# Optimization experiments

Measured on AMD Instinct MI355X. Metric: run time of the kernel, lower is better.

Reference implementation:

```python
import jax, jax.numpy as jnp
import numpy as np

C = 1.2            # PoincareBall curvature (learnable in torch, init value used)
SQC = C ** 0.5
MIN_NORM = 1e-15
BALL_EPS = 4e-3    # geoopt float32 projx eps

def _artanh(x):
    return jnp.arctanh(jnp.clip(x, -1.0 + 1e-7, 1.0 - 1e-7))

def _tanh(x):
    return jnp.tanh(jnp.clip(x, -15.0, 15.0))

def _norm(x):
    return jnp.maximum(jnp.linalg.norm(x, axis=-1, keepdims=True), MIN_NORM)

def p_projx(x):
    n = _norm(x)
    maxnorm = (1.0 - BALL_EPS) / SQC
    return jnp.where(n > maxnorm, x / n * maxnorm, x)

def p_expmap0(u):
    n = _norm(u)
    return p_projx(_tanh(SQC * n) * u / (SQC * n))

def p_logmap0(y):
    n = _norm(y)
    return _artanh(SQC * n) * y / (SQC * n)

def p_mobius_add(x, y):
    x2 = jnp.sum(x * x, -1, keepdims=True)
    y2 = jnp.sum(y * y, -1, keepdims=True)
    xy = jnp.sum(x * y, -1, keepdims=True)
    num = (1 + 2 * C * xy + C * y2) * x + (1 - C * x2) * y
    den = 1 + 2 * C * xy + C * C * x2 * y2
    return num / jnp.maximum(den, MIN_NORM)

def p_mobius_matvec(W, x):
    xn = _norm(x)
    mx = x @ W.T
    mxn = _norm(mx)
    res = _tanh(mxn / xn * _artanh(SQC * xn)) * mx / (mxn * SQC)
    zero = jnp.all(mx == 0, axis=-1, keepdims=True)
    return p_projx(jnp.where(zero, jnp.zeros_like(res), res))

def p_mobius_scalar_mul(r, x):
    n = _norm(x)
    return p_projx(_tanh(r * _artanh(SQC * n)) * x / (n * SQC))

def p_linear(x, W, b):
    # Manifold_Linear on PoincareBall: mobius matvec + mobius bias add + projx
    mv = p_mobius_matvec(W, x)
    return p_projx(p_mobius_add(mv, p_expmap0(b)))

def e_linear(x, W, b):
    return x @ W.T + b

def mob_relu(x):
    # Mob_Act: logmap0 -> act -> expmap0 (with projection)
    return p_expmap0(jax.nn.relu(p_logmap0(x)))


def setup_inputs() -> dict:
    key = jax.random.key(0)
    ks = jax.random.split(key, 26)
    g = lambda i, shape, s: (jax.random.normal(ks[i], shape, jnp.float32) * s)
    d = {
        'x':   g(0, (1024, 32, 128), 1.0),
        'We1': g(1, (80, 32), 0.1),   'be1': g(2, (80,), 0.05),
        'We2': g(3, (104, 80), 0.1),  'be2': g(4, (104,), 0.05),
        'We3': g(5, (128, 104), 0.1), 'be3': g(6, (128,), 0.05),
        'Wh1': g(7, (80, 32), 0.1),   'bh1': g(8, (80,), 0.05),
        'Wh2': g(9, (104, 80), 0.1),  'bh2': g(10, (104,), 0.05),
        'Wh3': g(11, (128, 104), 0.1),'bh3': g(12, (128,), 0.05),
        'Wae': g(13, (128, 128), 0.1),'bae': g(14, (128,), 0.05),
        'Wah': g(15, (128, 128), 0.1),'bah': g(16, (128,), 0.05),
        'Wte': g(17, (1, 128), 0.1),  'bte': g(18, (1,), 0.05),
        'Wth': g(19, (1, 128), 0.1),  'bth': g(20, (1,), 0.05),
        'Wf1': g(21, (10, 256), 0.1), 'bf1': g(22, (10,), 0.05),
        'Wf2': g(23, (10, 10), 0.1),  'bf2': g(24, (10,), 0.05),
    }
    return d


def reference(x, We1, be1, We2, be2, We3, be3,
              Wh1, bh1, Wh2, bh2, Wh3, bh3,
              Wae, bae, Wah, bah, Wte, bte, Wth, bth,
              Wf1, bf1, Wf2, bf2):
    xs = jnp.transpose(x, (0, 2, 1))  # (B, S, C_in)

    # --- Euclidean branch: expmap0 = identity; Manifold_Linear = plain linear ---
    xe = xs
    xe = e_linear(xe, We1, be1); xe = jax.nn.relu(xe)
    xe = e_linear(xe, We2, be2); xe = jax.nn.relu(xe)
    xe = e_linear(xe, We3, be3)
    out_e = jax.nn.relu(xe)               # extra self.act for Euclidean manifolds

    # --- Poincare branch ---
    xh = p_expmap0(xs)
    xh = p_linear(xh, Wh1, bh1); xh = mob_relu(xh)
    xh = p_linear(xh, Wh2, bh2); xh = mob_relu(xh)
    out_h = p_linear(xh, Wh3, bh3)        # (B, S, part_dim)

    # --- cross-manifold attention in tangent space at origin ---
    tan_e = e_linear(out_e, Wae, bae)                    # Euclidean logmap0 = id
    tan_h = p_logmap0(p_linear(out_h, Wah, bah))
    mu = 0.5 * (tan_e + tan_h)
    a_e = e_linear(tan_e - mu, Wte, bte)  # (B, S, 1)
    a_h = e_linear(tan_h - mu, Wth, bth)
    w = jax.nn.softmax(jnp.stack([a_e, a_h], axis=0), axis=0)
    proc_e = w[0] * out_e                                # Euclidean mobius scalar mul
    proc_h = p_mobius_scalar_mul(w[1], out_h)

    # --- pool over constituents in tangent space, concat, classify ---
    o_e = jnp.mean(proc_e, axis=1)                       # Euclidean logmap0 = id
    o_h = jnp.mean(p_logmap0(proc_h), axis=1)
    o = jnp.concatenate([o_e, o_h], axis=-1)             # (B, 2*part_dim)
    o = jax.nn.relu(e_linear(o, Wf1, bf1))
    return e_linear(o, Wf2, bf2)
```

## Files before the change

kernel.cpp:

```cpp
#include <hip/hip_runtime.h>
#include <math.h>

constexpr float CC   = 1.2f;
constexpr float SQC  = 1.09544511501033215f;
constexpr float MAXN = (1.0f - 4e-3f) / SQC;
constexpr float MINN = 1e-15f;

constexpr int WTH1 = 0;
constexpr int WTH2 = 4096;
constexpr int WTH3 = 14336;
constexpr int WTAH = 27648;
constexpr int WTE1 = 44032;
constexpr int WTE2 = 48128;
constexpr int WTE3 = 58368;
constexpr int EB1  = 71680;
constexpr int EB2  = 71808;
constexpr int EB3  = 71936;
constexpr int EBA  = 72064;
constexpr int BE1  = 72192;
constexpr int BE2  = 72320;
constexpr int BE3  = 72448;
constexpr int U1o  = 72576;
constexpr int U2o  = 72704;
constexpr int SCo  = 72832;
constexpr int PART = 72864;

constexpr int ASTR  = 65;
constexpr int L_ACT = 0;
constexpr int L_ZH  = 8320;
constexpr int L_SCR = 8960;
constexpr int L_TOT = 9000;

__device__ __forceinline__ float art_(float x){
  x = fminf(fmaxf(x, -0.9999999f), 0.9999999f);
  return 0.5f * __logf((1.0f + x) / (1.0f - x));
}
__device__ __forceinline__ float tanh_(float x){
  x = fminf(fmaxf(x, -15.0f), 15.0f);
  float e = __expf(2.0f * x);
  return (e - 1.0f) / (e + 1.0f);
}
__device__ __forceinline__ float wsum(float v){
#pragma unroll
  for(int i=32;i>0;i>>=1) v += __shfl_xor(v, i, 64);
  return v;
}
__device__ __forceinline__ float rtj(float v){
  v += __shfl_xor(v, 1, 64); v += __shfl_xor(v, 2, 64);
  v += __shfl_xor(v, 4, 64); v += __shfl_xor(v, 8, 64);
  return v;
}
__device__ __forceinline__ float lamv(float nv){
  float n = fmaxf(nv, MINN);
  return art_(SQC*n)/(SQC*n);
}
struct HS { float ca, cb, nv; };
__device__ __forceinline__ HS hyper_chain(float m2, float meb, float xn_in, float y2){
  float xn  = fmaxf(xn_in, MINN);
  float mxn = fmaxf(sqrtf(m2), MINN);
  float r   = art_(SQC*xn);
  float s   = tanh_(mxn/xn*r)/(mxn*SQC);
  float nr  = s*mxn;
  if(nr > MAXN){ s *= MAXN/nr; nr = MAXN; }
  float xy = s*meb, x2 = nr*nr;
  float den = fmaxf(1.f + 2.f*CC*xy + CC*CC*x2*y2, MINN);
  float A   = (1.f + 2.f*CC*xy + CC*y2)/den;
  float Bc  = (1.f - CC*x2)/den;
  float n3  = sqrtf(fmaxf(A*A*x2 + 2.f*A*Bc*xy + Bc*Bc*y2, 0.f));
  float rho = (n3 > MAXN) ? MAXN/n3 : 1.f;
  HS h; h.nv = fminf(n3, MAXN); h.ca = rho*A*s; h.cb = rho*Bc;
  return h;
}
struct TT { float tau, nf; };
__device__ __forceinline__ TT tail_relu(float rn2){
  float rn = fmaxf(sqrtf(rn2), MINN);
  float th = tanh_(SQC*rn);
  TT r; r.tau = th/(SQC*rn); r.nf = th/SQC;
  if(r.nf > MAXN){ r.tau *= MAXN/r.nf; r.nf = MAXN; }
  return r;
}
struct EX { float nh, scl; };
__device__ __forceinline__ EX exp0(float n2){
  float n0 = fmaxf(sqrtf(n2), MINN);
  float th = tanh_(SQC*n0);
  EX e; e.nh = th/SQC; e.scl = th/(SQC*n0);
  if(e.nh > MAXN){ e.scl *= MAXN/e.nh; e.nh = MAXN; }
  return e;
}
struct THW { float te, th2; };
__device__ __forceinline__ THW ahchain(float m2a, float mw1, float mw2, float meba,
                                       float xnh, float rr, float y2,
                                       float ebw1, float ebw2){
  float mxn = fmaxf(sqrtf(m2a), MINN);
  float s = tanh_(mxn/xnh*rr)/(mxn*SQC);
  float nr = s*mxn;
  if(nr > MAXN){ s *= MAXN/nr; nr = MAXN; }
  float xy = s*meba, x2 = nr*nr;
  float den = fmaxf(1.f + 2.f*CC*xy + CC*CC*x2*y2, MINN);
  float A = (1.f + 2.f*CC*xy + CC*y2)/den;
  float Bc = (1.f - CC*x2)/den;
  float n3 = sqrtf(fmaxf(A*A*x2 + 2.f*A*Bc*xy + Bc*Bc*y2, 0.f));
  float rho = (n3 > MAXN) ? MAXN/n3 : 1.f;
  float nv = fminf(n3, MAXN);
  float lr = lamv(nv)*rho;
  THW r; r.te = lr*(A*s*mw1 + Bc*ebw1); r.th2 = lr*(A*s*mw2 + Bc*ebw2);
  return r;
}
struct AG { float wge, g2; };
__device__ __forceinline__ AG attn(float d1, float d2, float thte, float thth,
                                   float rr, float xnh, float b_e, float b_h){
  float a_e = 0.5f*(d1 - thte) + b_e;
  float a_h = 0.5f*(thth - d2) + b_h;
  float mx = fmaxf(a_e, a_h);
  float ee = __expf(a_e - mx), eh = __expf(a_h - mx);
  float inv = 1.f/(ee + eh);
  AG r; r.wge = ee*inv;
  float wgh = eh*inv;
  float inner = wgh*rr;
  float scl2 = tanh_(inner)/(xnh*SQC);
  float nn = scl2*xnh;
  if(nn > MAXN){ scl2 *= MAXN/nn; nn = MAXN; }
  r.g2 = lamv(nn)*scl2;
  return r;
}

__global__ void k_setup(const float* __restrict__ Wh1, const float* __restrict__ Wh2,
                        const float* __restrict__ Wh3, const float* __restrict__ Wah,
                        const float* __restrict__ We1, const float* __restrict__ We2,
                        const float* __restrict__ We3,
                        const float* __restrict__ Wae, const float* __restrict__ bae,
                        const float* __restrict__ bh1, const float* __restrict__ bh2,
                        const float* __restrict__ bh3, const float* __restrict__ bah,
                        const float* __restrict__ Wte, const float* __restrict__ Wth,
                        const float* __restrict__ be1, const float* __restrict__ be2,
                        const float* __restrict__ be3, float* __restrict__ ws){
  const int blk = blockIdx.x, tid = threadIdx.x;
  if(blk < 280){
    const int row = blk*2 + (tid >> 7);
    const int j   = tid & 127;
    const float* W; int OUT, K, kk, dst;
    if(row < 32)       { W=Wh1; OUT=80;  K=32;  kk=row;      dst=WTH1; }
    else if(row < 112) { W=Wh2; OUT=104; K=80;  kk=row-32;   dst=WTH2; }
    else if(row < 216) { W=Wh3; OUT=128; K=104; kk=row-112;  dst=WTH3; }
    else if(row < 344) { W=Wah; OUT=128; K=128; kk=row-216;  dst=WTAH; }
    else if(row < 376) { W=We1; OUT=80;  K=32;  kk=row-344;  dst=WTE1; }
    else if(row < 456) { W=We2; OUT=104; K=80;  kk=row-376;  dst=WTE2; }
    else               { W=We3; OUT=128; K=104; kk=row-456;  dst=WTE3; }
    ws[dst + kk*128 + j] = (j < OUT) ? W[j*K + kk] : 0.f;
    return;
  }
  {
    const int which = tid >> 7, k = tid & 127;
    const float* wv = which ? Wth : Wte;
    float s = 0.f;
#pragma unroll 4
    for(int j=0;j<128;++j) s += Wae[j*128+k] * wv[j];
    ws[(which ? U2o : U1o) + k] = s;
  }
  if(tid < 128){
    ws[BE1+tid] = (tid < 80)  ? be1[tid] : 0.f;
    ws[BE2+tid] = (tid < 104) ? be2[tid] : 0.f;
    ws[BE3+tid] = be3[tid];
  }
  if(tid < 64){
    const int l = tid;
    float p1=0.f, p2=0.f;
    for(int j=l;j<128;j+=64){ p1 += bae[j]*Wte[j]; p2 += bae[j]*Wth[j]; }
    p1 = wsum(p1); p2 = wsum(p2);
    if(l==0){ ws[SCo+0]=p1; ws[SCo+1]=p2; }
    const float* bs[4] = {bh1,bh2,bh3,bah};
    const int dims[4]  = {80,104,128,128};
    const int offs[4]  = {EB1,EB2,EB3,EBA};
    for(int v=0;v<4;++v){
      const float* bp = bs[v]; const int D = dims[v];
      float q = 0.f;
      for(int j=l;j<D;j+=64) q += bp[j]*bp[j];
      q = wsum(q);
      float nb = fmaxf(sqrtf(q), MINN);
      float th = tanhf(fminf(fmaxf(SQC*nb,-15.f),15.f));
      float coef = th/(SQC*nb);
      float ne = th/SQC;
      if(ne > MAXN){ coef *= MAXN/ne; ne = MAXN; }
      for(int j=l;j<D;j+=64) ws[offs[v]+j] = coef*bp[j];
      for(int j=D+l;j<128;j+=64) ws[offs[v]+j] = 0.f;
      if(l==0) ws[SCo+2+v] = ne*ne;
      if(v==3){
        float e1=0.f, e2=0.f;
        for(int j=l;j<D;j+=64){ e1 += bp[j]*Wte[j]; e2 += bp[j]*Wth[j]; }
        e1 = wsum(e1)*coef; e2 = wsum(e2)*coef;
        if(l==0){ ws[SCo+6]=e1; ws[SCo+7]=e2; }
      }
    }
  }
}

__global__ void k_fin(const float* __restrict__ ws, const float* __restrict__ bf1,
                      const float* __restrict__ Wf2, const float* __restrict__ bf2,
                      float* __restrict__ out){
  const int r = blockIdx.x*64 + threadIdx.x;
  const float* p = ws + PART + (size_t)r*20;
  float f1[10];
#pragma unroll
  for(int i=0;i<10;++i)
    f1[i] = fmaxf((p[i] + p[10+i])*(1.f/128.f) + bf1[i], 0.f);
#pragma unroll
  for(int o=0;o<10;++o){
    float a = bf2[o];
#pragma unroll
    for(int k=0;k<10;++k) a = fmaf(Wf2[o*10+k], f1[k], a);
    out[r*10 + o] = a;
  }
}

__device__ __forceinline__ void ld8(const float* __restrict__ p, float (&v)[8]){
  float4 a = *(const float4*)p, b = *(const float4*)(p+4);
  v[0]=a.x; v[1]=a.y; v[2]=a.z; v[3]=a.w; v[4]=b.x; v[5]=b.y; v[6]=b.z; v[7]=b.w;
}

template<int K, bool XG, bool XSQ>
__device__ __forceinline__ void gemm4(const float* __restrict__ wt,
                                      const float* __restrict__ xg,
                                      const float* __restrict__ ACT,
                                      int tj, int tt, float (&acc)[4][8], float (&xsq)[4]){
#pragma unroll
  for(int i=0;i<4;++i)
#pragma unroll
    for(int j=0;j<8;++j) acc[i][j] = 0.f;
  const int wo = tj*8, xo = tt*4;
#pragma unroll 4
  for(int k=0;k<K;++k){
    float4 w0 = *(const float4*)(wt + k*128 + wo);
    float4 w1 = *(const float4*)(wt + k*128 + wo + 4);
    float4 xa;
    if(XG) xa = *(const float4*)(xg + k*128 + xo);
    else   xa = *(const float4*)(ACT + k*ASTR + xo);
    float xv[4] = {xa.x,xa.y,xa.z,xa.w};
    float wv[8] = {w0.x,w0.y,w0.z,w0.w,w1.x,w1.y,w1.z,w1.w};
#pragma unroll
    for(int i=0;i<4;++i){
      if(XSQ) xsq[i] = fmaf(xv[i], xv[i], xsq[i]);
#pragma unroll
      for(int j=0;j<8;++j) acc[i][j] = fmaf(xv[i], wv[j], acc[i][j]);
    }
  }
}

__device__ __forceinline__ void wACT(float* __restrict__ ACT, const float (&acc)[4][8],
                                     int tj, int tt){
#pragma unroll
  for(int j=0;j<8;++j){
    float4 a = {acc[0][j],acc[1][j],acc[2][j],acc[3][j]};
    *(float4*)(ACT + (tj*8+j)*ASTR + tt*4) = a;
  }
}

__global__ __launch_bounds__(256, 4) void k_main(
    const float* __restrict__ x,
    const float* __restrict__ Wf1, const float* __restrict__ Wte,
    const float* __restrict__ bte, const float* __restrict__ Wth,
    const float* __restrict__ bth, float* __restrict__ ws){
  extern __shared__ float lds[];
  float* ACT = lds + L_ACT;
  float* ZH  = lds + L_ZH;
  float* SCR = lds + L_SCR;
  const int tid = threadIdx.x, tj = tid & 15, tt = tid >> 4;
  const int b = blockIdx.x, b2 = b >> 1, hf = b & 1;
  const int tok0 = tt*4;
  const float* xg = x + (size_t)b2*4096 + hf*64;

  const float c1  = ws[SCo+0], c2  = ws[SCo+1];
  const float y21 = ws[SCo+2], y22 = ws[SCo+3], y23 = ws[SCo+4], y2a = ws[SCo+5];
  const float ew1 = ws[SCo+6], ew2 = ws[SCo+7];
  const float btev = bte[0], bthv = bth[0];

  float acc[4][8];
  float xsq[4];
#pragma unroll
  for(int i=0;i<4;++i) xsq[i] = 0.f;

  float nf[4], xnh[4], rr[4], tte[4], tth[4];

  {
    gemm4<32,true,true>(ws+WTH1, xg, ACT, tj, tt, acc, xsq);
    float ebv[8]; ld8(ws+EB1+tj*8, ebv);
#pragma unroll
    for(int i=0;i<4;++i){
      float s=0.f, e=0.f;
#pragma unroll
      for(int j=0;j<8;++j){ s = fmaf(acc[i][j],acc[i][j],s); e = fmaf(acc[i][j],ebv[j],e); }
      s = rtj(s); e = rtj(e);
      EX e0 = exp0(xsq[i]);
      HS h = hyper_chain(s*e0.scl*e0.scl, e*e0.scl, e0.nh, y21);
      float lam = lamv(h.nv), ca = h.ca*e0.scl, cb = h.cb;
      float s2 = 0.f;
#pragma unroll
      for(int j=0;j<8;++j){
        float v = fmaxf(lam*fmaf(ca, acc[i][j], cb*ebv[j]), 0.f);
        acc[i][j] = v; s2 = fmaf(v,v,s2);
      }
      s2 = rtj(s2);
      TT tr = tail_relu(s2); nf[i] = tr.nf;
#pragma unroll
      for(int j=0;j<8;++j) acc[i][j] *= tr.tau;
    }
    wACT(ACT, acc, tj, tt);
    __syncthreads();
  }

  {
    gemm4<80,false,false>(ws+WTH2, nullptr, ACT, tj, tt, acc, xsq);
    float ebv[8]; ld8(ws+EB2+tj*8, ebv);
#pragma unroll
    for(int i=0;i<4;++i){
      float s=0.f, e=0.f;
#pragma unroll
      for(int j=0;j<8;++j){ s = fmaf(acc[i][j],acc[i][j],s); e = fmaf(acc[i][j],ebv[j],e); }
      s = rtj(s); e = rtj(e);
      HS h = hyper_chain(s, e, nf[i], y22);
      float lam = lamv(h.nv);
      float s2 = 0.f;
#pragma unroll
      for(int j=0;j<8;++j){
        float v = fmaxf(lam*fmaf(h.ca, acc[i][j], h.cb*ebv[j]), 0.f);
        acc[i][j] = v; s2 = fmaf(v,v,s2);
      }
      s2 = rtj(s2);
      TT tr = tail_relu(s2); nf[i] = tr.nf;
#pragma unroll
      for(int j=0;j<8;++j) acc[i][j] *= tr.tau;
    }
    __syncthreads();
    wACT(ACT, acc, tj, tt);
    __syncthreads();
  }

  {
    gemm4<104,false,false>(ws+WTH3, nullptr, ACT, tj, tt, acc, xsq);
    float ebv[8]; ld8(ws+EB3+tj*8, ebv);
#pragma unroll
    for(int i=0;i<4;++i){
      float s=0.f, e=0.f;
#pragma unroll
      for(int j=0;j<8;++j){ s = fmaf(acc[i][j],acc[i][j],s); e = fmaf(acc[i][j],ebv[j],e); }
      s = rtj(s); e = rtj(e);
      HS h = hyper_chain(s, e, nf[i], y23);
      xnh[i] = fmaxf(h.nv, MINN);
      rr[i]  = art_(SQC*xnh[i]);
#pragma unroll
      for(int j=0;j<8;++j) acc[i][j] = fmaf(h.ca, acc[i][j], h.cb*ebv[j]);
    }
    __syncthreads();
    wACT(ACT, acc, tj, tt);
#pragma unroll
    for(int ic=0;ic<10;++ic){
      float wf[8]; ld8(Wf1 + ic*256 + 128 + tj*8, wf);
#pragma unroll
      for(int i=0;i<4;++i){
        float s=0.f;
#pragma unroll
        for(int j=0;j<8;++j) s = fmaf(acc[i][j], wf[j], s);
        s = rtj(s);
        if(tj==0) ZH[ic*64 + tok0 + i] = s;
      }
    }
    __syncthreads();
  }

  {
    gemm4<128,false,false>(ws+WTAH, nullptr, ACT, tj, tt, acc, xsq);
    float w1v[8], w2v[8], eav[8];
    ld8(Wte + tj*8, w1v); ld8(Wth + tj*8, w2v); ld8(ws+EBA+tj*8, eav);
#pragma unroll
    for(int i=0;i<4;++i){
      float s0=0.f,s1=0.f,s2=0.f,s3=0.f;
#pragma unroll
      for(int j=0;j<8;++j){
        float m = acc[i][j];
        s0 = fmaf(m,m,s0); s1 = fmaf(m,w1v[j],s1);
        s2 = fmaf(m,w2v[j],s2); s3 = fmaf(m,eav[j],s3);
      }
      s0=rtj(s0); s1=rtj(s1); s2=rtj(s2); s3=rtj(s3);
      THW a = ahchain(s0, s1, s2, s3, xnh[i], rr[i], y2a, ew1, ew2);
      tte[i] = a.te; tth[i] = a.th2;
    }
  }

  {
    gemm4<32,true,false>(ws+WTE1, xg, ACT, tj, tt, acc, xsq);
    float bev[8]; ld8(ws+BE1+tj*8, bev);
#pragma unroll
    for(int i=0;i<4;++i)
#pragma unroll
      for(int j=0;j<8;++j) acc[i][j] = fmaxf(acc[i][j]+bev[j], 0.f);
    __syncthreads();
    wACT(ACT, acc, tj, tt);
    __syncthreads();
  }
  {
    gemm4<80,false,false>(ws+WTE2, nullptr, ACT, tj, tt, acc, xsq);
    float bev[8]; ld8(ws+BE2+tj*8, bev);
#pragma unroll
    for(int i=0;i<4;++i)
#pragma unroll
      for(int j=0;j<8;++j) acc[i][j] = fmaxf(acc[i][j]+bev[j], 0.f);
    __syncthreads();
    wACT(ACT, acc, tj, tt);
    __syncthreads();
  }
  {
    gemm4<104,false,false>(ws+WTE3, nullptr, ACT, tj, tt, acc, xsq);
    float bev[8], u1v[8], u2v[8];
    ld8(ws+BE3+tj*8, bev); ld8(ws+U1o+tj*8, u1v); ld8(ws+U2o+tj*8, u2v);
    float wge[4], g2v[4];
#pragma unroll
    for(int i=0;i<4;++i){
      float s1=0.f, s2=0.f;
#pragma unroll
      for(int j=0;j<8;++j){
        float v = fmaxf(acc[i][j]+bev[j], 0.f);
        acc[i][j] = v;
        s1 = fmaf(v,u1v[j],s1); s2 = fmaf(v,u2v[j],s2);
      }
      s1 = rtj(s1); s2 = rtj(s2);
      AG g = attn(s1 + c1, s2 + c2, tte[i], tth[i], rr[i], xnh[i], btev, bthv);
      wge[i] = g.wge; g2v[i] = g.g2;
    }
#pragma unroll
    for(int ic=0;ic<10;++ic){
      float wf[8]; ld8(Wf1 + ic*256 + tj*8, wf);
      float pv = 0.f;
#pragma unroll
      for(int i=0;i<4;++i){
        float z=0.f;
#pragma unroll
        for(int j=0;j<8;++j) z = fmaf(acc[i][j], wf[j], z);
        z = rtj(z);
        pv += wge[i]*z + g2v[i]*ZH[ic*64 + tok0 + i];
      }
      pv += __shfl_xor(pv, 16, 64);
      pv += __shfl_xor(pv, 32, 64);
      if((tid & 63) == 0) SCR[(tid>>6)*10 + ic] = pv;
    }
    __syncthreads();
    if(tid < 10)
      ws[PART + (size_t)b*10 + tid] =
        SCR[tid] + SCR[10+tid] + SCR[20+tid] + SCR[30+tid];
  }
}

extern "C" void kernel_launch(void* const* d_in, const int* in_sizes, int n_in,
                              void* d_out, int out_size, void* d_ws, size_t ws_size,
                              hipStream_t stream){
  (void)in_sizes; (void)n_in; (void)out_size; (void)ws_size;
  const float* x   = (const float*)d_in[0];
  const float* We1 = (const float*)d_in[1];
  const float* be1 = (const float*)d_in[2];
  const float* We2 = (const float*)d_in[3];
  const float* be2 = (const float*)d_in[4];
  const float* We3 = (const float*)d_in[5];
  const float* be3 = (const float*)d_in[6];
  const float* Wh1 = (const float*)d_in[7];
  const float* bh1 = (const float*)d_in[8];
  const float* Wh2 = (const float*)d_in[9];
  const float* bh2 = (const float*)d_in[10];
  const float* Wh3 = (const float*)d_in[11];
  const float* bh3 = (const float*)d_in[12];
  const float* Wae = (const float*)d_in[13];
  const float* bae = (const float*)d_in[14];
  const float* Wah = (const float*)d_in[15];
  const float* bah = (const float*)d_in[16];
  const float* Wte = (const float*)d_in[17];
  const float* bte = (const float*)d_in[18];
  const float* Wth = (const float*)d_in[19];
  const float* bth = (const float*)d_in[20];
  const float* Wf1 = (const float*)d_in[21];
  const float* bf1 = (const float*)d_in[22];
  const float* Wf2 = (const float*)d_in[23];
  const float* bf2 = (const float*)d_in[24];
  float* ws  = (float*)d_ws;
  float* out = (float*)d_out;

  hipLaunchKernelGGL(k_setup, dim3(281), dim3(256), 0, stream,
                     Wh1, Wh2, Wh3, Wah, We1, We2, We3,
                     Wae, bae, bh1, bh2, bh3, bah, Wte, Wth, be1, be2, be3, ws);

  const int smem = L_TOT * 4;
  hipLaunchKernelGGL(k_main, dim3(2048), dim3(256), smem, stream,
                     x, Wf1, Wte, bte, Wth, bth, ws);

  hipLaunchKernelGGL(k_fin, dim3(16), dim3(64), 0, stream,
                     ws, bf1, Wf2, bf2, out);
}
```

Measured before the change: 590.8 us.

## Double threads per block with 4x4 register tiles and lane-distributed per-token chains

Blocks grow from 256 to 512 threads. Each thread now holds a 4x4 accumulator tile instead of 4x8, so output-feature reductions span 32 lanes. The per-token hyperbolic scalar chains, which every lane used to compute for all 4 of its tokens, now run once per lane for a single selected token, and the coefficients are broadcast back with shuffles. This spreads the expensive transcendental work and cuts register pressure to allow more resident waves, at the cost of extra shuffles and a longer reduction tree.

```diff
diff --git a/kernel.cpp b/kernel.cpp
--- a/kernel.cpp
+++ b/kernel.cpp
@@ -29,7 +29,7 @@
 constexpr int L_ACT = 0;
 constexpr int L_ZH  = 8320;
 constexpr int L_SCR = 8960;
-constexpr int L_TOT = 9000;
+constexpr int L_TOT = 9040;
 
 __device__ __forceinline__ float art_(float x){
   x = fminf(fmaxf(x, -0.9999999f), 0.9999999f);
@@ -45,11 +45,19 @@
   for(int i=32;i>0;i>>=1) v += __shfl_xor(v, i, 64);
   return v;
 }
-__device__ __forceinline__ float rtj(float v){
+__device__ __forceinline__ float rtj32(float v){
   v += __shfl_xor(v, 1, 64); v += __shfl_xor(v, 2, 64);
   v += __shfl_xor(v, 4, 64); v += __shfl_xor(v, 8, 64);
+  v += __shfl_xor(v, 16, 64);
   return v;
 }
+__device__ __forceinline__ float sel4(const float (&a)[4], int i){
+  float lo = (i & 1) ? a[1] : a[0];
+  float hi = (i & 1) ? a[3] : a[2];
+  return (i & 2) ? hi : lo;
+}
+__device__ __forceinline__ float bc(float v, int src){ return __shfl(v, src, 64); }
+
 __device__ __forceinline__ float lamv(float nv){
   float n = fmaxf(nv, MINN);
   return art_(SQC*n)/(SQC*n);
@@ -212,49 +220,48 @@
   }
 }
 
-__device__ __forceinline__ void ld8(const float* __restrict__ p, float (&v)[8]){
-  float4 a = *(const float4*)p, b = *(const float4*)(p+4);
-  v[0]=a.x; v[1]=a.y; v[2]=a.z; v[3]=a.w; v[4]=b.x; v[5]=b.y; v[6]=b.z; v[7]=b.w;
+__device__ __forceinline__ void ld4(const float* __restrict__ p, float (&v)[4]){
+  float4 a = *(const float4*)p;
+  v[0]=a.x; v[1]=a.y; v[2]=a.z; v[3]=a.w;
 }
 
 template<int K, bool XG, bool XSQ>
 __device__ __forceinline__ void gemm4(const float* __restrict__ wt,
                                       const float* __restrict__ xg,
                                       const float* __restrict__ ACT,
-                                      int tj, int tt, float (&acc)[4][8], float (&xsq)[4]){
+                                      int tj, int tt, float (&acc)[4][4], float (&xsq)[4]){
 #pragma unroll
   for(int i=0;i<4;++i)
 #pragma unroll
-    for(int j=0;j<8;++j) acc[i][j] = 0.f;
-  const int wo = tj*8, xo = tt*4;
+    for(int j=0;j<4;++j) acc[i][j] = 0.f;
+  const int wo = tj*4, xo = tt*4;
 #pragma unroll 4
   for(int k=0;k<K;++k){
-    float4 w0 = *(const float4*)(wt + k*128 + wo);
-    float4 w1 = *(const float4*)(wt + k*128 + wo + 4);
+    float4 w = *(const float4*)(wt + k*128 + wo);
     float4 xa;
     if(XG) xa = *(const float4*)(xg + k*128 + xo);
     else   xa = *(const float4*)(ACT + k*ASTR + xo);
     float xv[4] = {xa.x,xa.y,xa.z,xa.w};
-    float wv[8] = {w0.x,w0.y,w0.z,w0.w,w1.x,w1.y,w1.z,w1.w};
+    float wv[4] = {w.x,w.y,w.z,w.w};
 #pragma unroll
     for(int i=0;i<4;++i){
       if(XSQ) xsq[i] = fmaf(xv[i], xv[i], xsq[i]);
 #pragma unroll
-      for(int j=0;j<8;++j) acc[i][j] = fmaf(xv[i], wv[j], acc[i][j]);
-    }
-  }
-}
-
-__device__ __forceinline__ void wACT(float* __restrict__ ACT, const float (&acc)[4][8],
+      for(int j=0;j<4;++j) acc[i][j] = fmaf(xv[i], wv[j], acc[i][j]);
+    }
+  }
+}
+
+__device__ __forceinline__ void wACT(float* __restrict__ ACT, const float (&acc)[4][4],
                                      int tj, int tt){
 #pragma unroll
-  for(int j=0;j<8;++j){
+  for(int j=0;j<4;++j){
     float4 a = {acc[0][j],acc[1][j],acc[2][j],acc[3][j]};
-    *(float4*)(ACT + (tj*8+j)*ASTR + tt*4) = a;
-  }
-}
-
-__global__ __launch_bounds__(256, 4) void k_main(
+    *(float4*)(ACT + (tj*4+j)*ASTR + tt*4) = a;
+  }
+}
+
+__global__ __launch_bounds__(512, 8) void k_main(
     const float* __restrict__ x,
     const float* __restrict__ Wf1, const float* __restrict__ Wte,
     const float* __restrict__ bte, const float* __restrict__ Wth,
@@ -263,45 +270,53 @@
   float* ACT = lds + L_ACT;
   float* ZH  = lds + L_ZH;
   float* SCR = lds + L_SCR;
-  const int tid = threadIdx.x, tj = tid & 15, tt = tid >> 4;
+  const int tid = threadIdx.x, tj = tid & 31, tt = tid >> 5;
   const int b = blockIdx.x, b2 = b >> 1, hf = b & 1;
-  const int tok0 = tt*4;
+  const int i0 = tid & 3;
+  const int gb = tid & 32;
   const float* xg = x + (size_t)b2*4096 + hf*64;
 
-  const float c1  = ws[SCo+0], c2  = ws[SCo+1];
-  const float y21 = ws[SCo+2], y22 = ws[SCo+3], y23 = ws[SCo+4], y2a = ws[SCo+5];
-  const float ew1 = ws[SCo+6], ew2 = ws[SCo+7];
-  const float btev = bte[0], bthv = bth[0];
-
-  float acc[4][8];
+  float acc[4][4];
   float xsq[4];
 #pragma unroll
   for(int i=0;i<4;++i) xsq[i] = 0.f;
 
-  float nf[4], xnh[4], rr[4], tte[4], tth[4];
+  float nfO = 0.f, xnhO = 1.f, rrO = 0.f, tteO = 0.f, tthO = 0.f;
 
   {
     gemm4<32,true,true>(ws+WTH1, xg, ACT, tj, tt, acc, xsq);
-    float ebv[8]; ld8(ws+EB1+tj*8, ebv);
+    float ebv[4]; ld4(ws+EB1+tj*4, ebv);
+    float sA[4], eA[4];
 #pragma unroll
     for(int i=0;i<4;++i){
       float s=0.f, e=0.f;
 #pragma unroll
-      for(int j=0;j<8;++j){ s = fmaf(acc[i][j],acc[i][j],s); e = fmaf(acc[i][j],ebv[j],e); }
-      s = rtj(s); e = rtj(e);
-      EX e0 = exp0(xsq[i]);
-      HS h = hyper_chain(s*e0.scl*e0.scl, e*e0.scl, e0.nh, y21);
-      float lam = lamv(h.nv), ca = h.ca*e0.scl, cb = h.cb;
+      for(int j=0;j<4;++j){ s = fmaf(acc[i][j],acc[i][j],s); e = fmaf(acc[i][j],ebv[j],e); }
+      sA[i] = rtj32(s); eA[i] = rtj32(e);
+    }
+    EX e0 = exp0(sel4(xsq, i0));
+    HS h  = hyper_chain(sel4(sA,i0)*e0.scl*e0.scl, sel4(eA,i0)*e0.scl, e0.nh, ws[SCo+2]);
+    float lam = lamv(h.nv);
+    float Aw = lam*h.ca*e0.scl, Bw = lam*h.cb;
+    float s2A[4];
+#pragma unroll
+    for(int i=0;i<4;++i){
+      float Ab = bc(Aw, gb+i), Bb = bc(Bw, gb+i);
       float s2 = 0.f;
 #pragma unroll
-      for(int j=0;j<8;++j){
-        float v = fmaxf(lam*fmaf(ca, acc[i][j], cb*ebv[j]), 0.f);
+      for(int j=0;j<4;++j){
+        float v = fmaxf(fmaf(Ab, acc[i][j], Bb*ebv[j]), 0.f);
         acc[i][j] = v; s2 = fmaf(v,v,s2);
       }
-      s2 = rtj(s2);
-      TT tr = tail_relu(s2); nf[i] = tr.nf;
-#pragma unroll
-      for(int j=0;j<8;++j) acc[i][j] *= tr.tau;
+      s2A[i] = rtj32(s2);
+    }
+    TT tr = tail_relu(sel4(s2A, i0));
+    nfO = tr.nf;
+#pragma unroll
+    for(int i=0;i<4;++i){
+      float tb = bc(tr.tau, gb+i);
+#pragma unroll
+      for(int j=0;j<4;++j) acc[i][j] *= tb;
     }
     wACT(ACT, acc, tj, tt);
     __syncthreads();
@@ -309,25 +324,37 @@
 
   {
     gemm4<80,false,false>(ws+WTH2, nullptr, ACT, tj, tt, acc, xsq);
-    float ebv[8]; ld8(ws+EB2+tj*8, ebv);
+    float ebv[4]; ld4(ws+EB2+tj*4, ebv);
+    float sA[4], eA[4];
 #pragma unroll
     for(int i=0;i<4;++i){
       float s=0.f, e=0.f;
 #pragma unroll
-      for(int j=0;j<8;++j){ s = fmaf(acc[i][j],acc[i][j],s); e = fmaf(acc[i][j],ebv[j],e); }
-      s = rtj(s); e = rtj(e);
-      HS h = hyper_chain(s, e, nf[i], y22);
-      float lam = lamv(h.nv);
+      for(int j=0;j<4;++j){ s = fmaf(acc[i][j],acc[i][j],s); e = fmaf(acc[i][j],ebv[j],e); }
+      sA[i] = rtj32(s); eA[i] = rtj32(e);
+    }
+    HS h = hyper_chain(sel4(sA,i0), sel4(eA,i0), nfO, ws[SCo+3]);
+    float lam = lamv(h.nv);
+    float Aw = lam*h.ca, Bw = lam*h.cb;
+    float s2A[4];
+#pragma unroll
+    for(int i=0;i<4;++i){
+      float Ab = bc(Aw, gb+i), Bb = bc(Bw, gb+i);
       float s2 = 0.f;
 #pragma unroll
-      for(int j=0;j<8;++j){
-        float v = fmaxf(lam*fmaf(h.ca, acc[i][j], h.cb*ebv[j]), 0.f);
+      for(int j=0;j<4;++j){
+        float v = fmaxf(fmaf(Ab, acc[i][j], Bb*ebv[j]), 0.f);
         acc[i][j] = v; s2 = fmaf(v,v,s2);
       }
-      s2 = rtj(s2);
-      TT tr = tail_relu(s2); nf[i] = tr.nf;
-#pragma unroll
-      for(int j=0;j<8;++j) acc[i][j] *= tr.tau;
+      s2A[i] = rtj32(s2);
+    }
+    TT tr = tail_relu(sel4(s2A, i0));
+    nfO = tr.nf;
+#pragma unroll
+    for(int i=0;i<4;++i){
+      float tb = bc(tr.tau, gb+i);
+#pragma unroll
+      for(int j=0;j<4;++j) acc[i][j] *= tb;
     }
     __syncthreads();
     wACT(ACT, acc, tj, tt);
@@ -336,31 +363,36 @@
 
   {
     gemm4<104,false,false>(ws+WTH3, nullptr, ACT, tj, tt, acc, xsq);
-    float ebv[8]; ld8(ws+EB3+tj*8, ebv);
+    float ebv[4]; ld4(ws+EB3+tj*4, ebv);
+    float sA[4], eA[4];
 #pragma unroll
     for(int i=0;i<4;++i){
       float s=0.f, e=0.f;
 #pragma unroll
-      for(int j=0;j<8;++j){ s = fmaf(acc[i][j],acc[i][j],s); e = fmaf(acc[i][j],ebv[j],e); }
-      s = rtj(s); e = rtj(e);
-      HS h = hyper_chain(s, e, nf[i], y23);
-      xnh[i] = fmaxf(h.nv, MINN);
-      rr[i]  = art_(SQC*xnh[i]);
-#pragma unroll
-      for(int j=0;j<8;++j) acc[i][j] = fmaf(h.ca, acc[i][j], h.cb*ebv[j]);
+      for(int j=0;j<4;++j){ s = fmaf(acc[i][j],acc[i][j],s); e = fmaf(acc[i][j],ebv[j],e); }
+      sA[i] = rtj32(s); eA[i] = rtj32(e);
+    }
+    HS h = hyper_chain(sel4(sA,i0), sel4(eA,i0), nfO, ws[SCo+4]);
+    xnhO = fmaxf(h.nv, MINN);
+    rrO  = art_(SQC*xnhO);
+#pragma unroll
+    for(int i=0;i<4;++i){
+      float ca = bc(h.ca, gb+i), cb = bc(h.cb, gb+i);
+#pragma unroll
+      for(int j=0;j<4;++j) acc[i][j] = fmaf(ca, acc[i][j], cb*ebv[j]);
     }
     __syncthreads();
     wACT(ACT, acc, tj, tt);
 #pragma unroll
     for(int ic=0;ic<10;++ic){
-      float wf[8]; ld8(Wf1 + ic*256 + 128 + tj*8, wf);
+      float wf[4]; ld4(Wf1 + ic*256 + 128 + tj*4, wf);
 #pragma unroll
       for(int i=0;i<4;++i){
         float s=0.f;
 #pragma unroll
-        for(int j=0;j<8;++j) s = fmaf(acc[i][j], wf[j], s);
-        s = rtj(s);
-        if(tj==0) ZH[ic*64 + tok0 + i] = s;
+        for(int j=0;j<4;++j) s = fmaf(acc[i][j], wf[j], s);
+        s = rtj32(s);
+        if(tj==0) ZH[ic*64 + tt*4 + i] = s;
       }
     }
     __syncthreads();
@@ -368,83 +400,90 @@
 
   {
     gemm4<128,false,false>(ws+WTAH, nullptr, ACT, tj, tt, acc, xsq);
-    float w1v[8], w2v[8], eav[8];
-    ld8(Wte + tj*8, w1v); ld8(Wth + tj*8, w2v); ld8(ws+EBA+tj*8, eav);
+    float w1v[4], w2v[4], eav[4];
+    ld4(Wte + tj*4, w1v); ld4(Wth + tj*4, w2v); ld4(ws+EBA+tj*4, eav);
+    float aA[4], bA[4], cA[4], dA[4];
 #pragma unroll
     for(int i=0;i<4;++i){
       float s0=0.f,s1=0.f,s2=0.f,s3=0.f;
 #pragma unroll
-      for(int j=0;j<8;++j){
+      for(int j=0;j<4;++j){
         float m = acc[i][j];
         s0 = fmaf(m,m,s0); s1 = fmaf(m,w1v[j],s1);
         s2 = fmaf(m,w2v[j],s2); s3 = fmaf(m,eav[j],s3);
       }
-      s0=rtj(s0); s1=rtj(s1); s2=rtj(s2); s3=rtj(s3);
-      THW a = ahchain(s0, s1, s2, s3, xnh[i], rr[i], y2a, ew1, ew2);
-      tte[i] = a.te; tth[i] = a.th2;
-    }
+      aA[i]=rtj32(s0); bA[i]=rtj32(s1); cA[i]=rtj32(s2); dA[i]=rtj32(s3);
+    }
+    THW a = ahchain(sel4(aA,i0), sel4(bA,i0), sel4(cA,i0), sel4(dA,i0),
+                    xnhO, rrO, ws[SCo+5], ws[SCo+6], ws[SCo+7]);
+    tteO = a.te; tthO = a.th2;
   }
 
   {
     gemm4<32,true,false>(ws+WTE1, xg, ACT, tj, tt, acc, xsq);
-    float bev[8]; ld8(ws+BE1+tj*8, bev);
+    float bev[4]; ld4(ws+BE1+tj*4, bev);
 #pragma unroll
     for(int i=0;i<4;++i)
 #pragma unroll
-      for(int j=0;j<8;++j) acc[i][j] = fmaxf(acc[i][j]+bev[j], 0.f);
+      for(int j=0;j<4;++j) acc[i][j] = fmaxf(acc[i][j]+bev[j], 0.f);
     __syncthreads();
     wACT(ACT, acc, tj, tt);
     __syncthreads();
   }
   {
     gemm4<80,false,false>(ws+WTE2, nullptr, ACT, tj, tt, acc, xsq);
-    float bev[8]; ld8(ws+BE2+tj*8, bev);
+    float bev[4]; ld4(ws+BE2+tj*4, bev);
 #pragma unroll
     for(int i=0;i<4;++i)
 #pragma unroll
-      for(int j=0;j<8;++j) acc[i][j] = fmaxf(acc[i][j]+bev[j], 0.f);
+      for(int j=0;j<4;++j) acc[i][j] = fmaxf(acc[i][j]+bev[j], 0.f);
     __syncthreads();
     wACT(ACT, acc, tj, tt);
     __syncthreads();
   }
   {
     gemm4<104,false,false>(ws+WTE3, nullptr, ACT, tj, tt, acc, xsq);
-    float bev[8], u1v[8], u2v[8];
-    ld8(ws+BE3+tj*8, bev); ld8(ws+U1o+tj*8, u1v); ld8(ws+U2o+tj*8, u2v);
-    float wge[4], g2v[4];
+    float bev[4], u1v[4], u2v[4];
+    ld4(ws+BE3+tj*4, bev); ld4(ws+U1o+tj*4, u1v); ld4(ws+U2o+tj*4, u2v);
+    float s1A[4], s2A[4];
 #pragma unroll
     for(int i=0;i<4;++i){
       float s1=0.f, s2=0.f;
 #pragma unroll
-      for(int j=0;j<8;++j){
+      for(int j=0;j<4;++j){
         float v = fmaxf(acc[i][j]+bev[j], 0.f);
         acc[i][j] = v;
         s1 = fmaf(v,u1v[j],s1); s2 = fmaf(v,u2v[j],s2);
       }
-      s1 = rtj(s1); s2 = rtj(s2);
-      AG g = attn(s1 + c1, s2 + c2, tte[i], tth[i], rr[i], xnh[i], btev, bthv);
-      wge[i] = g.wge; g2v[i] = g.g2;
-    }
+      s1A[i] = rtj32(s1); s2A[i] = rtj32(s2);
+    }
+    AG g = attn(sel4(s1A,i0) + ws[SCo+0], sel4(s2A,i0) + ws[SCo+1],
+                tteO, tthO, rrO, xnhO, bte[0], bth[0]);
+    float wb[4], g2b[4];
+#pragma unroll
+    for(int i=0;i<4;++i){ wb[i] = bc(g.wge, gb+i); g2b[i] = bc(g.g2, gb+i); }
 #pragma unroll
     for(int ic=0;ic<10;++ic){
-      float wf[8]; ld8(Wf1 + ic*256 + tj*8, wf);
+      float wf[4]; ld4(Wf1 + ic*256 + tj*4, wf);
       float pv = 0.f;
 #pragma unroll
       for(int i=0;i<4;++i){
         float z=0.f;
 #pragma unroll
-        for(int j=0;j<8;++j) z = fmaf(acc[i][j], wf[j], z);
-        z = rtj(z);
-        pv += wge[i]*z + g2v[i]*ZH[ic*64 + tok0 + i];
-      }
-      pv += __shfl_xor(pv, 16, 64);
+        for(int j=0;j<4;++j) z = fmaf(acc[i][j], wf[j], z);
+        z = rtj32(z);
+        pv += wb[i]*z + g2b[i]*ZH[ic*64 + tt*4 + i];
+      }
       pv += __shfl_xor(pv, 32, 64);
       if((tid & 63) == 0) SCR[(tid>>6)*10 + ic] = pv;
     }
     __syncthreads();
-    if(tid < 10)
-      ws[PART + (size_t)b*10 + tid] =
-        SCR[tid] + SCR[10+tid] + SCR[20+tid] + SCR[30+tid];
+    if(tid < 10){
+      float s = 0.f;
+#pragma unroll
+      for(int w=0;w<8;++w) s += SCR[w*10 + tid];
+      ws[PART + (size_t)b*10 + tid] = s;
+    }
   }
 }
 
@@ -485,7 +524,7 @@
                      Wae, bae, bh1, bh2, bh3, bah, Wte, Wth, be1, be2, be3, ws);
 
   const int smem = L_TOT * 4;
-  hipLaunchKernelGGL(k_main, dim3(2048), dim3(256), smem, stream,
+  hipLaunchKernelGGL(k_main, dim3(2048), dim3(512), smem, stream,
                      x, Wf1, Wte, bte, Wth, bth, ws);
 
   hipLaunchKernelGGL(k_fin, dim3(16), dim3(64), 0, stream,
```

New measurement: 965.8 us. +63.5%, slower.

## Shrink main kernel to single-wave blocks to drop barriers and redundant scalar chains

Applied to the files above, without the earlier changes.

Each block now covers 16 tokens with one 64-lane wavefront instead of 64 tokens with four waves, so the grid grows to 8192 blocks and every __syncthreads disappears. The per-token hyperbolic scalar chains are computed once per token by a designated lane (chosen with sel4) and broadcast with shuffles, instead of being recomputed by all 16 lanes sharing that token. The ZH/SCR shared staging is replaced by registers and a wave reduction, and k_fin sums 8 partials per row instead of 2. In exchange, each block does much less work, so launch and scheduling overhead is larger, the weight-tile reads from global/L2 are reused across only 16 tokens instead of 64, and dropping the barriers relies on same-wave ordering of LDS accesses.

```diff
diff --git a/kernel.cpp b/kernel.cpp
--- a/kernel.cpp
+++ b/kernel.cpp
@@ -25,11 +25,7 @@
 constexpr int SCo  = 72832;
 constexpr int PART = 72864;
 
-constexpr int ASTR  = 65;
-constexpr int L_ACT = 0;
-constexpr int L_ZH  = 8320;
-constexpr int L_SCR = 8960;
-constexpr int L_TOT = 9000;
+constexpr int ASTR = 17;
 
 __device__ __forceinline__ float art_(float x){
   x = fminf(fmaxf(x, -0.9999999f), 0.9999999f);
@@ -49,6 +45,14 @@
   v += __shfl_xor(v, 1, 64); v += __shfl_xor(v, 2, 64);
   v += __shfl_xor(v, 4, 64); v += __shfl_xor(v, 8, 64);
   return v;
+}
+__device__ __forceinline__ float sel4(const float (&a)[4], int i){
+  float lo = (i & 1) ? a[1] : a[0];
+  float hi = (i & 1) ? a[3] : a[2];
+  return (i & 2) ? hi : lo;
+}
+__device__ __forceinline__ float bcx(float v, int tid, int i){
+  return __shfl(v, (tid & 60) | i, 64);
 }
 __device__ __forceinline__ float lamv(float nv){
   float n = fmaxf(nv, MINN);
@@ -198,11 +202,15 @@
                       const float* __restrict__ Wf2, const float* __restrict__ bf2,
                       float* __restrict__ out){
   const int r = blockIdx.x*64 + threadIdx.x;
-  const float* p = ws + PART + (size_t)r*20;
+  const float* p = ws + PART + (size_t)r*80;
   float f1[10];
 #pragma unroll
-  for(int i=0;i<10;++i)
-    f1[i] = fmaxf((p[i] + p[10+i])*(1.f/128.f) + bf1[i], 0.f);
+  for(int i=0;i<10;++i){
+    float s = 0.f;
+#pragma unroll
+    for(int g=0;g<8;++g) s += p[g*10+i];
+    f1[i] = fmaxf(s*(1.f/512.f) + bf1[i], 0.f);
+  }
 #pragma unroll
   for(int o=0;o<10;++o){
     float a = bf2[o];
@@ -218,15 +226,15 @@
 }
 
 template<int K, bool XG, bool XSQ>
-__device__ __forceinline__ void gemm4(const float* __restrict__ wt,
+__device__ __forceinline__ void gemmw(const float* __restrict__ wt,
                                       const float* __restrict__ xg,
                                       const float* __restrict__ ACT,
-                                      int tj, int tt, float (&acc)[4][8], float (&xsq)[4]){
+                                      int fj, int tt, float (&acc)[4][8], float (&xsq)[4]){
 #pragma unroll
   for(int i=0;i<4;++i)
 #pragma unroll
     for(int j=0;j<8;++j) acc[i][j] = 0.f;
-  const int wo = tj*8, xo = tt*4;
+  const int wo = fj*8, xo = tt*4;
 #pragma unroll 4
   for(int k=0;k<K;++k){
     float4 w0 = *(const float4*)(wt + k*128 + wo);
@@ -246,27 +254,24 @@
 }
 
 __device__ __forceinline__ void wACT(float* __restrict__ ACT, const float (&acc)[4][8],
-                                     int tj, int tt){
+                                     int fj, int tt){
 #pragma unroll
   for(int j=0;j<8;++j){
     float4 a = {acc[0][j],acc[1][j],acc[2][j],acc[3][j]};
-    *(float4*)(ACT + (tj*8+j)*ASTR + tt*4) = a;
-  }
-}
-
-__global__ __launch_bounds__(256, 4) void k_main(
+    *(float4*)(ACT + (fj*8+j)*ASTR + tt*4) = a;
+  }
+}
+
+__global__ __launch_bounds__(64) void k_main(
     const float* __restrict__ x,
     const float* __restrict__ Wf1, const float* __restrict__ Wte,
     const float* __restrict__ bte, const float* __restrict__ Wth,
     const float* __restrict__ bth, float* __restrict__ ws){
-  extern __shared__ float lds[];
-  float* ACT = lds + L_ACT;
-  float* ZH  = lds + L_ZH;
-  float* SCR = lds + L_SCR;
-  const int tid = threadIdx.x, tj = tid & 15, tt = tid >> 4;
-  const int b = blockIdx.x, b2 = b >> 1, hf = b & 1;
-  const int tok0 = tt*4;
-  const float* xg = x + (size_t)b2*4096 + hf*64;
+  __shared__ float ACT[128*ASTR];
+  const int tid = threadIdx.x, fj = tid & 15, tt = tid >> 4;
+  const int b = blockIdx.x, row = b >> 3, q = b & 7;
+  const int own = fj & 3;
+  const float* xg = x + (size_t)row*4096 + q*16;
 
   const float c1  = ws[SCo+0], c2  = ws[SCo+1];
   const float y21 = ws[SCo+2], y22 = ws[SCo+3], y23 = ws[SCo+4], y2a = ws[SCo+5];
@@ -278,98 +283,125 @@
 #pragma unroll
   for(int i=0;i<4;++i) xsq[i] = 0.f;
 
-  float nf[4], xnh[4], rr[4], tte[4], tth[4];
-
-  {
-    gemm4<32,true,true>(ws+WTH1, xg, ACT, tj, tt, acc, xsq);
-    float ebv[8]; ld8(ws+EB1+tj*8, ebv);
+  float nfO = 0.f, xnhO = 1.f, rrO = 0.f, tteO = 0.f, tthO = 0.f;
+  float zhO[10];
+
+  {
+    gemmw<32,true,true>(ws+WTH1, xg, ACT, fj, tt, acc, xsq);
+    float ebv[8]; ld8(ws+EB1+fj*8, ebv);
+    float sA[4], eA[4];
 #pragma unroll
     for(int i=0;i<4;++i){
       float s=0.f, e=0.f;
 #pragma unroll
       for(int j=0;j<8;++j){ s = fmaf(acc[i][j],acc[i][j],s); e = fmaf(acc[i][j],ebv[j],e); }
-      s = rtj(s); e = rtj(e);
-      EX e0 = exp0(xsq[i]);
-      HS h = hyper_chain(s*e0.scl*e0.scl, e*e0.scl, e0.nh, y21);
-      float lam = lamv(h.nv), ca = h.ca*e0.scl, cb = h.cb;
+      sA[i] = rtj(s); eA[i] = rtj(e);
+    }
+    EX e0 = exp0(sel4(xsq, own));
+    HS h  = hyper_chain(sel4(sA,own)*e0.scl*e0.scl, sel4(eA,own)*e0.scl, e0.nh, y21);
+    float lam = lamv(h.nv);
+    float Aw = lam*h.ca*e0.scl, Bw = lam*h.cb;
+    float s2A[4];
+#pragma unroll
+    for(int i=0;i<4;++i){
+      float Ab = bcx(Aw,tid,i), Bb = bcx(Bw,tid,i);
       float s2 = 0.f;
 #pragma unroll
       for(int j=0;j<8;++j){
-        float v = fmaxf(lam*fmaf(ca, acc[i][j], cb*ebv[j]), 0.f);
+        float v = fmaxf(fmaf(Ab, acc[i][j], Bb*ebv[j]), 0.f);
         acc[i][j] = v; s2 = fmaf(v,v,s2);
       }
-      s2 = rtj(s2);
-      TT tr = tail_relu(s2); nf[i] = tr.nf;
-#pragma unroll
-      for(int j=0;j<8;++j) acc[i][j] *= tr.tau;
-    }
-    wACT(ACT, acc, tj, tt);
-    __syncthreads();
-  }
-
-  {
-    gemm4<80,false,false>(ws+WTH2, nullptr, ACT, tj, tt, acc, xsq);
-    float ebv[8]; ld8(ws+EB2+tj*8, ebv);
+      s2A[i] = rtj(s2);
+    }
+    TT tr = tail_relu(sel4(s2A, own));
+    nfO = tr.nf;
+#pragma unroll
+    for(int i=0;i<4;++i){
+      float tb = bcx(tr.tau,tid,i);
+#pragma unroll
+      for(int j=0;j<8;++j) acc[i][j] *= tb;
+    }
+    wACT(ACT, acc, fj, tt);
+  }
+
+  {
+    gemmw<80,false,false>(ws+WTH2, nullptr, ACT, fj, tt, acc, xsq);
+    float ebv[8]; ld8(ws+EB2+fj*8, ebv);
+    float sA[4], eA[4];
 #pragma unroll
     for(int i=0;i<4;++i){
       float s=0.f, e=0.f;
 #pragma unroll
       for(int j=0;j<8;++j){ s = fmaf(acc[i][j],acc[i][j],s); e = fmaf(acc[i][j],ebv[j],e); }
-      s = rtj(s); e = rtj(e);
-      HS h = hyper_chain(s, e, nf[i], y22);
-      float lam = lamv(h.nv);
+      sA[i] = rtj(s); eA[i] = rtj(e);
+    }
+    HS h = hyper_chain(sel4(sA,own), sel4(eA,own), nfO, y22);
+    float lam = lamv(h.nv);
+    float Aw = lam*h.ca, Bw = lam*h.cb;
+    float s2A[4];
+#pragma unroll
+    for(int i=0;i<4;++i){
+      float Ab = bcx(Aw,tid,i), Bb = bcx(Bw,tid,i);
       float s2 = 0.f;
 #pragma unroll
       for(int j=0;j<8;++j){
-        float v = fmaxf(lam*fmaf(h.ca, acc[i][j], h.cb*ebv[j]), 0.f);
+        float v = fmaxf(fmaf(Ab, acc[i][j], Bb*ebv[j]), 0.f);
         acc[i][j] = v; s2 = fmaf(v,v,s2);
       }
-      s2 = rtj(s2);
-      TT tr = tail_relu(s2); nf[i] = tr.nf;
-#pragma unroll
-      for(int j=0;j<8;++j) acc[i][j] *= tr.tau;
-    }
-    __syncthreads();
-    wACT(ACT, acc, tj, tt);
-    __syncthreads();
-  }
-
-  {
-    gemm4<104,false,false>(ws+WTH3, nullptr, ACT, tj, tt, acc, xsq);
-    float ebv[8]; ld8(ws+EB3+tj*8, ebv);
+      s2A[i] = rtj(s2);
+    }
+    TT tr = tail_relu(sel4(s2A, own));
+    nfO = tr.nf;
+#pragma unroll
+    for(int i=0;i<4;++i){
+      float tb = bcx(tr.tau,tid,i);
+#pragma unroll
+      for(int j=0;j<8;++j) acc[i][j] *= tb;
+    }
+    wACT(ACT, acc, fj, tt);
+  }
+
+  {
+    gemmw<104,false,false>(ws+WTH3, nullptr, ACT, fj, tt, acc, xsq);
+    float ebv[8]; ld8(ws+EB3+fj*8, ebv);
+    float sA[4], eA[4];
 #pragma unroll
     for(int i=0;i<4;++i){
       float s=0.f, e=0.f;
 #pragma unroll
       for(int j=0;j<8;++j){ s = fmaf(acc[i][j],acc[i][j],s); e = fmaf(acc[i][j],ebv[j],e); }
-      s = rtj(s); e = rtj(e);
-      HS h = hyper_chain(s, e, nf[i], y23);
-      xnh[i] = fmaxf(h.nv, MINN);
-      rr[i]  = art_(SQC*xnh[i]);
-#pragma unroll
-      for(int j=0;j<8;++j) acc[i][j] = fmaf(h.ca, acc[i][j], h.cb*ebv[j]);
-    }
-    __syncthreads();
-    wACT(ACT, acc, tj, tt);
+      sA[i] = rtj(s); eA[i] = rtj(e);
+    }
+    HS h = hyper_chain(sel4(sA,own), sel4(eA,own), nfO, y23);
+    xnhO = fmaxf(h.nv, MINN);
+    rrO  = art_(SQC*xnhO);
+#pragma unroll
+    for(int i=0;i<4;++i){
+      float ca = bcx(h.ca,tid,i), cb = bcx(h.cb,tid,i);
+#pragma unroll
+      for(int j=0;j<8;++j) acc[i][j] = fmaf(ca, acc[i][j], cb*ebv[j]);
+    }
+    wACT(ACT, acc, fj, tt);
 #pragma unroll
     for(int ic=0;ic<10;++ic){
-      float wf[8]; ld8(Wf1 + ic*256 + 128 + tj*8, wf);
+      float wf[8]; ld8(Wf1 + ic*256 + 128 + fj*8, wf);
+      float zA[4];
 #pragma unroll
       for(int i=0;i<4;++i){
         float s=0.f;
 #pragma unroll
         for(int j=0;j<8;++j) s = fmaf(acc[i][j], wf[j], s);
-        s = rtj(s);
-        if(tj==0) ZH[ic*64 + tok0 + i] = s;
-      }
-    }
-    __syncthreads();
-  }
-
-  {
-    gemm4<128,false,false>(ws+WTAH, nullptr, ACT, tj, tt, acc, xsq);
+        zA[i] = rtj(s);
+      }
+      zhO[ic] = sel4(zA, own);
+    }
+  }
+
+  {
+    gemmw<128,false,false>(ws+WTAH, nullptr, ACT, fj, tt, acc, xsq);
     float w1v[8], w2v[8], eav[8];
-    ld8(Wte + tj*8, w1v); ld8(Wth + tj*8, w2v); ld8(ws+EBA+tj*8, eav);
+    ld8(Wte + fj*8, w1v); ld8(Wth + fj*8, w2v); ld8(ws+EBA+fj*8, eav);
+    float aA[4], bA[4], cA[4], dA[4];
 #pragma unroll
     for(int i=0;i<4;++i){
       float s0=0.f,s1=0.f,s2=0.f,s3=0.f;
@@ -379,39 +411,36 @@
         s0 = fmaf(m,m,s0); s1 = fmaf(m,w1v[j],s1);
         s2 = fmaf(m,w2v[j],s2); s3 = fmaf(m,eav[j],s3);
       }
-      s0=rtj(s0); s1=rtj(s1); s2=rtj(s2); s3=rtj(s3);
-      THW a = ahchain(s0, s1, s2, s3, xnh[i], rr[i], y2a, ew1, ew2);
-      tte[i] = a.te; tth[i] = a.th2;
-    }
-  }
-
-  {
-    gemm4<32,true,false>(ws+WTE1, xg, ACT, tj, tt, acc, xsq);
-    float bev[8]; ld8(ws+BE1+tj*8, bev);
+      aA[i]=rtj(s0); bA[i]=rtj(s1); cA[i]=rtj(s2); dA[i]=rtj(s3);
+    }
+    THW a = ahchain(sel4(aA,own), sel4(bA,own), sel4(cA,own), sel4(dA,own),
+                    xnhO, rrO, y2a, ew1, ew2);
+    tteO = a.te; tthO = a.th2;
+  }
+
+  {
+    gemmw<32,true,false>(ws+WTE1, xg, ACT, fj, tt, acc, xsq);
+    float bev[8]; ld8(ws+BE1+fj*8, bev);
 #pragma unroll
     for(int i=0;i<4;++i)
 #pragma unroll
       for(int j=0;j<8;++j) acc[i][j] = fmaxf(acc[i][j]+bev[j], 0.f);
-    __syncthreads();
-    wACT(ACT, acc, tj, tt);
-    __syncthreads();
-  }
-  {
-    gemm4<80,false,false>(ws+WTE2, nullptr, ACT, tj, tt, acc, xsq);
-    float bev[8]; ld8(ws+BE2+tj*8, bev);
+    wACT(ACT, acc, fj, tt);
+  }
+  {
+    gemmw<80,false,false>(ws+WTE2, nullptr, ACT, fj, tt, acc, xsq);
+    float bev[8]; ld8(ws+BE2+fj*8, bev);
 #pragma unroll
     for(int i=0;i<4;++i)
 #pragma unroll
       for(int j=0;j<8;++j) acc[i][j] = fmaxf(acc[i][j]+bev[j], 0.f);
-    __syncthreads();
-    wACT(ACT, acc, tj, tt);
-    __syncthreads();
-  }
-  {
-    gemm4<104,false,false>(ws+WTE3, nullptr, ACT, tj, tt, acc, xsq);
+    wACT(ACT, acc, fj, tt);
+  }
+  {
+    gemmw<104,false,false>(ws+WTE3, nullptr, ACT, fj, tt, acc, xsq);
     float bev[8], u1v[8], u2v[8];
-    ld8(ws+BE3+tj*8, bev); ld8(ws+U1o+tj*8, u1v); ld8(ws+U2o+tj*8, u2v);
-    float wge[4], g2v[4];
+    ld8(ws+BE3+fj*8, bev); ld8(ws+U1o+fj*8, u1v); ld8(ws+U2o+fj*8, u2v);
+    float s1A[4], s2A[4];
 #pragma unroll
     for(int i=0;i<4;++i){
       float s1=0.f, s2=0.f;
@@ -421,30 +450,25 @@
         acc[i][j] = v;
         s1 = fmaf(v,u1v[j],s1); s2 = fmaf(v,u2v[j],s2);
       }
-      s1 = rtj(s1); s2 = rtj(s2);
-      AG g = attn(s1 + c1, s2 + c2, tte[i], tth[i], rr[i], xnh[i], btev, bthv);
-      wge[i] = g.wge; g2v[i] = g.g2;
-    }
+      s1A[i] = rtj(s1); s2A[i] = rtj(s2);
+    }
+    AG g = attn(sel4(s1A,own) + c1, sel4(s2A,own) + c2,
+                tteO, tthO, rrO, xnhO, btev, bthv);
 #pragma unroll
     for(int ic=0;ic<10;++ic){
-      float wf[8]; ld8(Wf1 + ic*256 + tj*8, wf);
-      float pv = 0.f;
+      float wf[8]; ld8(Wf1 + ic*256 + fj*8, wf);
+      float zA[4];
 #pragma unroll
       for(int i=0;i<4;++i){
-        float z=0.f;
-#pragma unroll
-        for(int j=0;j<8;++j) z = fmaf(acc[i][j], wf[j], z);
-        z = rtj(z);
-        pv += wge[i]*z + g2v[i]*ZH[ic*64 + tok0 + i];
-      }
-      pv += __shfl_xor(pv, 16, 64);
-      pv += __shfl_xor(pv, 32, 64);
-      if((tid & 63) == 0) SCR[(tid>>6)*10 + ic] = pv;
-    }
-    __syncthreads();
-    if(tid < 10)
-      ws[PART + (size_t)b*10 + tid] =
-        SCR[tid] + SCR[10+tid] + SCR[20+tid] + SCR[30+tid];
+        float s=0.f;
+#pragma unroll
+        for(int j=0;j<8;++j) s = fmaf(acc[i][j], wf[j], s);
+        zA[i] = rtj(s);
+      }
+      float p = g.wge*sel4(zA,own) + g.g2*zhO[ic];
+      p = wsum(p);
+      if(tid == 0) ws[PART + (size_t)b*10 + ic] = p;
+    }
   }
 }
 
@@ -484,8 +508,7 @@
                      Wh1, Wh2, Wh3, Wah, We1, We2, We3,
                      Wae, bae, bh1, bh2, bh3, bah, Wte, Wth, be1, be2, be3, ws);
 
-  const int smem = L_TOT * 4;
-  hipLaunchKernelGGL(k_main, dim3(2048), dim3(256), smem, stream,
+  hipLaunchKernelGGL(k_main, dim3(8192), dim3(64), 0, stream,
                      x, Wf1, Wte, bte, Wth, bth, ws);
 
   hipLaunchKernelGGL(k_fin, dim3(16), dim3(64), 0, stream,
```

After: 568.2 us. 3.8% less time.
